# Optimization experiments

Measured on AMD Instinct MI355X. Metric: run time of the kernel, lower is better.

The kernel has to match this reference:

```python
import jax, jax.numpy as jnp
import numpy as np


def setup_inputs() -> dict:
    key = jax.random.key(0)
    kq, kk, kv = jax.random.split(key, 3)
    B, S, D = 4, 4096, 64
    q = jax.random.normal(kq, (B, S, D), dtype=jnp.float32)
    k = jax.random.normal(kk, (B, S, D), dtype=jnp.float32)
    v = jax.random.normal(kv, (B, S, D), dtype=jnp.float32)
    return {"q": q, "k": k, "v": v}


def reference(q, k, v):
    # q,k,v: [B,S,D]. Faithful to the torch module:
    #   attn = softmax(q @ k^T / sqrt(D))  -- softmax over full row (NOT pre-masked)
    #   attn = attn.masked_fill(tril==0, 0.0)  -- post-softmax causal zeroing
    #   out  = attn @ v
    S = q.shape[1]
    d = jnp.sqrt(jnp.asarray(q.shape[-1], dtype=q.dtype))
    scores = jnp.einsum("bqd,bkd->bqk", q, k) / d  # [B,S,S]
    attn = jax.nn.softmax(scores, axis=-1)
    # causal tril mask sliced from the registered buffer mask[:S,:S]
    causal = jnp.tril(jnp.ones((S, S), dtype=bool))  # [S,S]
    attn = jnp.where(causal[None, :, :], attn, jnp.asarray(0.0, dtype=attn.dtype))
    out = jnp.einsum("bqk,bkd->bqd", attn, v)  # [B,S,D]
    return out
```

## Files before the change

### kernel.cpp

```cpp
#include <hip/hip_runtime.h>
#include <math.h>


typedef _Float16 f16;
typedef __attribute__((ext_vector_type(8))) _Float16 f16x8;
typedef __attribute__((ext_vector_type(16))) float f32x16;
typedef __attribute__((ext_vector_type(4))) unsigned int uint4x;

constexpr int S = 4096, D = 64, TK = 32;
constexpr int B_ = 4;
constexpr int NKT = S / TK;
constexpr int WPB = 4;
constexpr int TPW = NKT / WPB;
constexpr float QSC = 0.125f * 1.44269504088896340736f;

__global__ __launch_bounds__(256) void prep(
    const float* __restrict__ K, const float* __restrict__ V,
    f16* __restrict__ Kfrag, f16* __restrict__ Vfrag) {
  const int bx = blockIdx.x, tid = threadIdx.x;
  if (bx < B_ * NKT) {
    const float* src = K + (size_t)bx * TK * D;
    const int key = tid >> 3, j = tid & 7;
    float4 f0 = *reinterpret_cast<const float4*>(src + key * D + j * 8);
    float4 f1 = *reinterpret_cast<const float4*>(src + key * D + j * 8 + 4);
    f16x8 h;
    h[0] = (f16)f0.x; h[1] = (f16)f0.y; h[2] = (f16)f0.z; h[3] = (f16)f0.w;
    h[4] = (f16)f1.x; h[5] = (f16)f1.y; h[6] = (f16)f1.z; h[7] = (f16)f1.w;
    const int kc = j >> 1, h2 = j & 1;
    const int lane = key + 32 * h2;
    *reinterpret_cast<f16x8*>(Kfrag + ((size_t)bx * 4 + kc) * 512 + lane * 8) = h;
  } else {
    __shared__ float t32[TK][D + 4];
    const int vb = bx - B_ * NKT;
    const float* src = V + (size_t)vb * TK * D;
    #pragma unroll
    for (int r = 0; r < 2; ++r) {
      int f4 = tid + r * 256;
      int row = f4 >> 4, c4 = (f4 & 15) * 4;
      *reinterpret_cast<float4*>(&t32[row][c4]) =
          *reinterpret_cast<const float4*>(src + row * D + c4);
    }
    __syncthreads();
    const int dn = tid >> 7, kc2 = (tid >> 6) & 1, lane = tid & 63;
    const int l31 = lane & 31, h2 = lane >> 5;
    const int dim = dn * 32 + l31;
    const int k0 = kc2 * 16 + 8 * h2;
    f16x8 h;
    #pragma unroll
    for (int jj = 0; jj < 8; ++jj) h[jj] = (f16)t32[k0 + jj][dim];
    *reinterpret_cast<f16x8*>(
        Vfrag + ((size_t)vb * 4 + dn * 2 + kc2) * 512 + lane * 8) = h;
  }
}

__global__ __launch_bounds__(256, 3)
void attn(const float* __restrict__ Q, const f16* __restrict__ Kfrag,
          const f16* __restrict__ Vfrag, float* __restrict__ O) {
  __shared__ struct { float nb[2][32][68]; float db[WPB][32]; } sm;

  const int i = blockIdx.x;
  const int b = (i & 7) >> 1;
  const int t = ((i >> 3) << 1) | (i & 1);
  const int qb = (t & 1) ? (127 - (t >> 1)) : (t >> 1);
  const int q0 = qb * TK;

  const int tid = threadIdx.x;
  const int w = tid >> 6, lane = tid & 63;
  const int l31 = lane & 31, h2 = lane >> 5;

  const size_t bSD = (size_t)b * S * D;

  f16x8 qh[4], qlo[4];
  {
    const float* qr = Q + bSD + (size_t)(q0 + l31) * D;
    #pragma unroll
    for (int kc = 0; kc < 4; ++kc) {
      float4 f0 = *reinterpret_cast<const float4*>(qr + kc * 16 + 8 * h2);
      float4 f1 = *reinterpret_cast<const float4*>(qr + kc * 16 + 8 * h2 + 4);
      float f[8] = {f0.x, f0.y, f0.z, f0.w, f1.x, f1.y, f1.z, f1.w};
      #pragma unroll
      for (int j = 0; j < 8; ++j) {
        float v = f[j] * QSC;
        f16 hi = (f16)v;
        qh[kc][j] = hi;
        qlo[kc][j] = (f16)(v - (float)hi);
      }
    }
  }

  const f16* kf = Kfrag + (size_t)b * NKT * 2048 + lane * 8;
  const f16* vf = Vfrag + (size_t)b * NKT * 2048 + lane * 8;

  f32x16 on0, on1;
  float dv[4];
  #pragma unroll
  for (int r = 0; r < 16; ++r) { on0[r] = 0.f; on1[r] = 0.f; }
  #pragma unroll
  for (int r = 0; r < 4; ++r) dv[r] = 0.f;

  f16x8 bk0, bk1, bk2, bk3;
  {
    const f16* kp = kf + (size_t)w * 2048;
    bk0 = *reinterpret_cast<const f16x8*>(kp);
    bk1 = *reinterpret_cast<const f16x8*>(kp + 512);
    bk2 = *reinterpret_cast<const f16x8*>(kp + 1024);
    bk3 = *reinterpret_cast<const f16x8*>(kp + 1536);
  }

  for (int j = 0; j < TPW; ++j) {
    const int kt = (j << 2) | w;
    const int kbase = kt * TK;
    const bool pv = (kbase <= q0);
    const bool diag = (kbase == q0);

    f16x8 v00, v01, v10, v11;
    if (pv) {
      const f16* vp = vf + (size_t)kt * 2048;
      v00 = *reinterpret_cast<const f16x8*>(vp);
      v01 = *reinterpret_cast<const f16x8*>(vp + 512);
      v10 = *reinterpret_cast<const f16x8*>(vp + 1024);
      v11 = *reinterpret_cast<const f16x8*>(vp + 1536);
    }

    f16x8 kn0, kn1, kn2, kn3;
    if (j + 1 < TPW) {
      const f16* kpn = kf + ((size_t)kt + 4) * 2048;
      kn0 = *reinterpret_cast<const f16x8*>(kpn);
      kn1 = *reinterpret_cast<const f16x8*>(kpn + 512);
      kn2 = *reinterpret_cast<const f16x8*>(kpn + 1024);
      kn3 = *reinterpret_cast<const f16x8*>(kpn + 1536);
    }

    f32x16 acc;
    #pragma unroll
    for (int r = 0; r < 16; ++r) acc[r] = 0.f;
    acc = __builtin_amdgcn_mfma_f32_32x32x16_f16(bk0, qlo[0], acc, 0, 0, 0);
    acc = __builtin_amdgcn_mfma_f32_32x32x16_f16(bk0, qh[0],  acc, 0, 0, 0);
    acc = __builtin_amdgcn_mfma_f32_32x32x16_f16(bk1, qlo[1], acc, 0, 0, 0);
    acc = __builtin_amdgcn_mfma_f32_32x32x16_f16(bk1, qh[1],  acc, 0, 0, 0);
    acc = __builtin_amdgcn_mfma_f32_32x32x16_f16(bk2, qlo[2], acc, 0, 0, 0);
    acc = __builtin_amdgcn_mfma_f32_32x32x16_f16(bk2, qh[2],  acc, 0, 0, 0);
    acc = __builtin_amdgcn_mfma_f32_32x32x16_f16(bk3, qlo[3], acc, 0, 0, 0);
    acc = __builtin_amdgcn_mfma_f32_32x32x16_f16(bk3, qh[3],  acc, 0, 0, 0);

    if (pv) {
      unsigned pw[8];
      const int kb4 = 4 * h2;
      #pragma unroll
      for (int i2 = 0; i2 < 8; ++i2) {
        const int ra = 2 * i2, rb = ra + 1;
        float pa = __builtin_amdgcn_exp2f(acc[ra]);
        float pb = __builtin_amdgcn_exp2f(acc[rb]);
        f16 ha = (f16)pa, hb = (f16)pb;
        dv[i2 & 3] += (float)ha + (float)hb;
        unsigned short ba = __builtin_bit_cast(unsigned short, ha);
        unsigned short bb = __builtin_bit_cast(unsigned short, hb);
        if (diag) {
          const int kra = (ra & 3) + 8 * (ra >> 2) + kb4;
          const int krb = (rb & 3) + 8 * (rb >> 2) + kb4;
          ba = (kra <= l31) ? ba : (unsigned short)0;
          bb = (krb <= l31) ? bb : (unsigned short)0;
        }
        pw[i2] = (unsigned)ba | ((unsigned)bb << 16);
      }
      asm("v_permlane32_swap_b32 %0, %1" : "+v"(pw[0]), "+v"(pw[2]));
      asm("v_permlane32_swap_b32 %0, %1" : "+v"(pw[1]), "+v"(pw[3]));
      asm("v_permlane32_swap_b32 %0, %1" : "+v"(pw[4]), "+v"(pw[6]));
      asm("v_permlane32_swap_b32 %0, %1" : "+v"(pw[5]), "+v"(pw[7]));
      uint4x u0 = {pw[0], pw[1], pw[2], pw[3]};
      uint4x u1 = {pw[4], pw[5], pw[6], pw[7]};
      f16x8 ap0 = __builtin_bit_cast(f16x8, u0);
      f16x8 ap1 = __builtin_bit_cast(f16x8, u1);

      on0 = __builtin_amdgcn_mfma_f32_32x32x16_f16(ap0, v00, on0, 0, 0, 0);
      on0 = __builtin_amdgcn_mfma_f32_32x32x16_f16(ap1, v01, on0, 0, 0, 0);
      on1 = __builtin_amdgcn_mfma_f32_32x32x16_f16(ap0, v10, on1, 0, 0, 0);
      on1 = __builtin_amdgcn_mfma_f32_32x32x16_f16(ap1, v11, on1, 0, 0, 0);
    } else {
      #pragma unroll
      for (int r = 0; r < 16; ++r) dv[r & 3] += __builtin_amdgcn_exp2f(acc[r]);
    }

    bk0 = kn0; bk1 = kn1; bk2 = kn2; bk3 = kn3;
  }

  float den = dv[0] + dv[1] + dv[2] + dv[3];
  den += __shfl_xor(den, 32);
  if (h2 == 0) sm.db[w][l31] = den;

  if (w < 2) {
    #pragma unroll
    for (int r = 0; r < 16; ++r) {
      const int row = (r & 3) + 8 * (r >> 2) + 4 * h2;
      sm.nb[w][row][l31]      = on0[r];
      sm.nb[w][row][32 + l31] = on1[r];
    }
  }
  __syncthreads();
  if (w >= 2) {
    #pragma unroll
    for (int r = 0; r < 16; ++r) {
      const int row = (r & 3) + 8 * (r >> 2) + 4 * h2;
      sm.nb[w - 2][row][l31]      += on0[r];
      sm.nb[w - 2][row][32 + l31] += on1[r];
    }
  }
  __syncthreads();

  #pragma unroll
  for (int it = 0; it < 2; ++it) {
    const int i4 = tid + it * 256;
    const int row = i4 >> 4, c4 = (i4 & 15) * 4;
    float dsum = 0.f;
    #pragma unroll
    for (int ww = 0; ww < WPB; ++ww) dsum += sm.db[ww][row];
    const float inv = 1.f / dsum;
    float4 a0 = *reinterpret_cast<const float4*>(&sm.nb[0][row][c4]);
    float4 a1 = *reinterpret_cast<const float4*>(&sm.nb[1][row][c4]);
    float4 o;
    o.x = (a0.x + a1.x) * inv;
    o.y = (a0.y + a1.y) * inv;
    o.z = (a0.z + a1.z) * inv;
    o.w = (a0.w + a1.w) * inv;
    *reinterpret_cast<float4*>(O + bSD + (size_t)(q0 + row) * D + c4) = o;
  }
}

extern "C" void kernel_launch(void* const* d_in, const int* in_sizes, int n_in,
                              void* d_out, int out_size, void* d_ws, size_t ws_size,
                              hipStream_t stream) {
  const float* q = (const float*)d_in[0];
  const float* k = (const float*)d_in[1];
  const float* v = (const float*)d_in[2];
  float* o = (float*)d_out;

  f16* Kfrag = (f16*)d_ws;
  f16* Vfrag = Kfrag + (size_t)B_ * S * D;

  prep<<<dim3(2 * B_ * NKT), dim3(256), 0, stream>>>(k, v, Kfrag, Vfrag);
  attn<<<dim3(512), dim3(256), 0, stream>>>(q, Kfrag, Vfrag, o);
}
```

Measured before the change: 94.22 us.

## Pair early and late query tiles per block so K/V fragments are shared

Each block now handles two query tiles, qb and 127-qb, with 8 waves of 64 lanes instead of 4. Each loaded K/V fragment feeds both tiles' QK^T and PV MFMAs, which halves K/V global traffic per query and balances causal work inside each block. The cost is doubled accumulator registers, a 512-thread launch bound with 2 blocks per CU, only 256 blocks, and a longer shared-memory reduction epilogue with extra barriers.

```diff
diff --git a/kernel.cpp b/kernel.cpp
--- a/kernel.cpp
+++ b/kernel.cpp
@@ -10,7 +10,7 @@
 constexpr int S = 4096, D = 64, TK = 32;
 constexpr int B_ = 4;
 constexpr int NKT = S / TK;
-constexpr int WPB = 4;
+constexpr int WPB = 8;
 constexpr int TPW = NKT / WPB;
 constexpr float QSC = 0.125f * 1.44269504088896340736f;
 
@@ -53,25 +53,31 @@
   }
 }
 
-__global__ __launch_bounds__(256, 3)
+__global__ __launch_bounds__(512, 2)
 void attn(const float* __restrict__ Q, const f16* __restrict__ Kfrag,
           const f16* __restrict__ Vfrag, float* __restrict__ O) {
-  __shared__ struct { float nb[2][32][68]; float db[WPB][32]; } sm;
+  __shared__ struct {
+    float nb[4][32][68];
+    float db[2][8][32];
+  } sm;
 
   const int i = blockIdx.x;
   const int b = (i & 7) >> 1;
-  const int t = ((i >> 3) << 1) | (i & 1);
-  const int qb = (t & 1) ? (127 - (t >> 1)) : (t >> 1);
-  const int q0 = qb * TK;
+  const int qb = ((i >> 3) << 1) | (i & 1);
+  const int qbB = 127 - qb;
+  const int q0A = qb * TK, q0B = qbB * TK;
 
   const int tid = threadIdx.x;
   const int w = tid >> 6, lane = tid & 63;
   const int l31 = lane & 31, h2 = lane >> 5;
+  const int kb4 = 4 * h2;
 
   const size_t bSD = (size_t)b * S * D;
 
-  f16x8 qh[4], qlo[4];
-  {
+  f16x8 qh[2][4], qlo[2][4];
+  #pragma unroll
+  for (int t = 0; t < 2; ++t) {
+    const int q0 = t ? q0B : q0A;
     const float* qr = Q + bSD + (size_t)(q0 + l31) * D;
     #pragma unroll
     for (int kc = 0; kc < 4; ++kc) {
@@ -82,8 +88,8 @@
       for (int j = 0; j < 8; ++j) {
         float v = f[j] * QSC;
         f16 hi = (f16)v;
-        qh[kc][j] = hi;
-        qlo[kc][j] = (f16)(v - (float)hi);
+        qh[t][kc][j] = hi;
+        qlo[t][kc][j] = (f16)(v - (float)hi);
       }
     }
   }
@@ -91,12 +97,50 @@
   const f16* kf = Kfrag + (size_t)b * NKT * 2048 + lane * 8;
   const f16* vf = Vfrag + (size_t)b * NKT * 2048 + lane * 8;
 
-  f32x16 on0, on1;
-  float dv[4];
+  f32x16 onA0, onA1, onB0, onB1;
+  float dvA[4], dvB[4];
   #pragma unroll
-  for (int r = 0; r < 16; ++r) { on0[r] = 0.f; on1[r] = 0.f; }
+  for (int r = 0; r < 16; ++r) {
+    onA0[r] = 0.f; onA1[r] = 0.f; onB0[r] = 0.f; onB1[r] = 0.f;
+  }
   #pragma unroll
-  for (int r = 0; r < 4; ++r) dv[r] = 0.f;
+  for (int r = 0; r < 4; ++r) { dvA[r] = 0.f; dvB[r] = 0.f; }
+
+  auto sm_pv = [&](const f32x16& acc, bool diag, float* dv,
+                   f32x16& o0, f32x16& o1,
+                   const f16x8& v00, const f16x8& v01,
+                   const f16x8& v10, const f16x8& v11) {
+    unsigned pw[8];
+    #pragma unroll
+    for (int i2 = 0; i2 < 8; ++i2) {
+      const int ra = 2 * i2, rb = ra + 1;
+      float pa = __builtin_amdgcn_exp2f(acc[ra]);
+      float pb = __builtin_amdgcn_exp2f(acc[rb]);
+      f16 ha = (f16)pa, hb = (f16)pb;
+      dv[i2 & 3] += (float)ha + (float)hb;
+      unsigned short ba = __builtin_bit_cast(unsigned short, ha);
+      unsigned short bb = __builtin_bit_cast(unsigned short, hb);
+      if (diag) {
+        const int kra = (ra & 3) + 8 * (ra >> 2) + kb4;
+        const int krb = (rb & 3) + 8 * (rb >> 2) + kb4;
+        ba = (kra <= l31) ? ba : (unsigned short)0;
+        bb = (krb <= l31) ? bb : (unsigned short)0;
+      }
+      pw[i2] = (unsigned)ba | ((unsigned)bb << 16);
+    }
+    asm("v_permlane32_swap_b32 %0, %1" : "+v"(pw[0]), "+v"(pw[2]));
+    asm("v_permlane32_swap_b32 %0, %1" : "+v"(pw[1]), "+v"(pw[3]));
+    asm("v_permlane32_swap_b32 %0, %1" : "+v"(pw[4]), "+v"(pw[6]));
+    asm("v_permlane32_swap_b32 %0, %1" : "+v"(pw[5]), "+v"(pw[7]));
+    uint4x u0 = {pw[0], pw[1], pw[2], pw[3]};
+    uint4x u1 = {pw[4], pw[5], pw[6], pw[7]};
+    f16x8 ap0 = __builtin_bit_cast(f16x8, u0);
+    f16x8 ap1 = __builtin_bit_cast(f16x8, u1);
+    o0 = __builtin_amdgcn_mfma_f32_32x32x16_f16(ap0, v00, o0, 0, 0, 0);
+    o0 = __builtin_amdgcn_mfma_f32_32x32x16_f16(ap1, v01, o0, 0, 0, 0);
+    o1 = __builtin_amdgcn_mfma_f32_32x32x16_f16(ap0, v10, o1, 0, 0, 0);
+    o1 = __builtin_amdgcn_mfma_f32_32x32x16_f16(ap1, v11, o1, 0, 0, 0);
+  };
 
   f16x8 bk0, bk1, bk2, bk3;
   {
@@ -108,13 +152,12 @@
   }
 
   for (int j = 0; j < TPW; ++j) {
-    const int kt = (j << 2) | w;
-    const int kbase = kt * TK;
-    const bool pv = (kbase <= q0);
-    const bool diag = (kbase == q0);
+    const int kt = (j << 3) | w;
+    const bool pvA = (kt <= qb),  diagA = (kt == qb);
+    const bool pvB = (kt <= qbB), diagB = (kt == qbB);
 
     f16x8 v00, v01, v10, v11;
-    if (pv) {
+    if (pvB) {
       const f16* vp = vf + (size_t)kt * 2048;
       v00 = *reinterpret_cast<const f16x8*>(vp);
       v01 = *reinterpret_cast<const f16x8*>(vp + 512);
@@ -124,105 +167,133 @@
 
     f16x8 kn0, kn1, kn2, kn3;
     if (j + 1 < TPW) {
-      const f16* kpn = kf + ((size_t)kt + 4) * 2048;
+      const f16* kpn = kf + ((size_t)kt + WPB) * 2048;
       kn0 = *reinterpret_cast<const f16x8*>(kpn);
       kn1 = *reinterpret_cast<const f16x8*>(kpn + 512);
       kn2 = *reinterpret_cast<const f16x8*>(kpn + 1024);
       kn3 = *reinterpret_cast<const f16x8*>(kpn + 1536);
     }
 
-    f32x16 acc;
-    #pragma unroll
-    for (int r = 0; r < 16; ++r) acc[r] = 0.f;
-    acc = __builtin_amdgcn_mfma_f32_32x32x16_f16(bk0, qlo[0], acc, 0, 0, 0);
-    acc = __builtin_amdgcn_mfma_f32_32x32x16_f16(bk0, qh[0],  acc, 0, 0, 0);
-    acc = __builtin_amdgcn_mfma_f32_32x32x16_f16(bk1, qlo[1], acc, 0, 0, 0);
-    acc = __builtin_amdgcn_mfma_f32_32x32x16_f16(bk1, qh[1],  acc, 0, 0, 0);
-    acc = __builtin_amdgcn_mfma_f32_32x32x16_f16(bk2, qlo[2], acc, 0, 0, 0);
-    acc = __builtin_amdgcn_mfma_f32_32x32x16_f16(bk2, qh[2],  acc, 0, 0, 0);
-    acc = __builtin_amdgcn_mfma_f32_32x32x16_f16(bk3, qlo[3], acc, 0, 0, 0);
-    acc = __builtin_amdgcn_mfma_f32_32x32x16_f16(bk3, qh[3],  acc, 0, 0, 0);
-
-    if (pv) {
-      unsigned pw[8];
-      const int kb4 = 4 * h2;
+    {
+      f32x16 acc;
       #pragma unroll
-      for (int i2 = 0; i2 < 8; ++i2) {
-        const int ra = 2 * i2, rb = ra + 1;
-        float pa = __builtin_amdgcn_exp2f(acc[ra]);
-        float pb = __builtin_amdgcn_exp2f(acc[rb]);
-        f16 ha = (f16)pa, hb = (f16)pb;
-        dv[i2 & 3] += (float)ha + (float)hb;
-        unsigned short ba = __builtin_bit_cast(unsigned short, ha);
-        unsigned short bb = __builtin_bit_cast(unsigned short, hb);
-        if (diag) {
-          const int kra = (ra & 3) + 8 * (ra >> 2) + kb4;
-          const int krb = (rb & 3) + 8 * (rb >> 2) + kb4;
-          ba = (kra <= l31) ? ba : (unsigned short)0;
-          bb = (krb <= l31) ? bb : (unsigned short)0;
-        }
-        pw[i2] = (unsigned)ba | ((unsigned)bb << 16);
+      for (int r = 0; r < 16; ++r) acc[r] = 0.f;
+      acc = __builtin_amdgcn_mfma_f32_32x32x16_f16(bk0, qlo[0][0], acc, 0, 0, 0);
+      acc = __builtin_amdgcn_mfma_f32_32x32x16_f16(bk0, qh[0][0],  acc, 0, 0, 0);
+      acc = __builtin_amdgcn_mfma_f32_32x32x16_f16(bk1, qlo[0][1], acc, 0, 0, 0);
+      acc = __builtin_amdgcn_mfma_f32_32x32x16_f16(bk1, qh[0][1],  acc, 0, 0, 0);
+      acc = __builtin_amdgcn_mfma_f32_32x32x16_f16(bk2, qlo[0][2], acc, 0, 0, 0);
+      acc = __builtin_amdgcn_mfma_f32_32x32x16_f16(bk2, qh[0][2],  acc, 0, 0, 0);
+      acc = __builtin_amdgcn_mfma_f32_32x32x16_f16(bk3, qlo[0][3], acc, 0, 0, 0);
+      acc = __builtin_amdgcn_mfma_f32_32x32x16_f16(bk3, qh[0][3],  acc, 0, 0, 0);
+      if (pvA) {
+        sm_pv(acc, diagA, dvA, onA0, onA1, v00, v01, v10, v11);
+      } else {
+        #pragma unroll
+        for (int r = 0; r < 16; ++r) dvA[r & 3] += __builtin_amdgcn_exp2f(acc[r]);
       }
-      asm("v_permlane32_swap_b32 %0, %1" : "+v"(pw[0]), "+v"(pw[2]));
-      asm("v_permlane32_swap_b32 %0, %1" : "+v"(pw[1]), "+v"(pw[3]));
-      asm("v_permlane32_swap_b32 %0, %1" : "+v"(pw[4]), "+v"(pw[6]));
-      asm("v_permlane32_swap_b32 %0, %1" : "+v"(pw[5]), "+v"(pw[7]));
-      uint4x u0 = {pw[0], pw[1], pw[2], pw[3]};
-      uint4x u1 = {pw[4], pw[5], pw[6], pw[7]};
-      f16x8 ap0 = __builtin_bit_cast(f16x8, u0);
-      f16x8 ap1 = __builtin_bit_cast(f16x8, u1);
-
-      on0 = __builtin_amdgcn_mfma_f32_32x32x16_f16(ap0, v00, on0, 0, 0, 0);
-      on0 = __builtin_amdgcn_mfma_f32_32x32x16_f16(ap1, v01, on0, 0, 0, 0);
-      on1 = __builtin_amdgcn_mfma_f32_32x32x16_f16(ap0, v10, on1, 0, 0, 0);
-      on1 = __builtin_amdgcn_mfma_f32_32x32x16_f16(ap1, v11, on1, 0, 0, 0);
-    } else {
+    }
+
+    {
+      f32x16 acc;
       #pragma unroll
-      for (int r = 0; r < 16; ++r) dv[r & 3] += __builtin_amdgcn_exp2f(acc[r]);
+      for (int r = 0; r < 16; ++r) acc[r] = 0.f;
+      acc = __builtin_amdgcn_mfma_f32_32x32x16_f16(bk0, qlo[1][0], acc, 0, 0, 0);
+      acc = __builtin_amdgcn_mfma_f32_32x32x16_f16(bk0, qh[1][0],  acc, 0, 0, 0);
+      acc = __builtin_amdgcn_mfma_f32_32x32x16_f16(bk1, qlo[1][1], acc, 0, 0, 0);
+      acc = __builtin_amdgcn_mfma_f32_32x32x16_f16(bk1, qh[1][1],  acc, 0, 0, 0);
+      acc = __builtin_amdgcn_mfma_f32_32x32x16_f16(bk2, qlo[1][2], acc, 0, 0, 0);
+      acc = __builtin_amdgcn_mfma_f32_32x32x16_f16(bk2, qh[1][2],  acc, 0, 0, 0);
+      acc = __builtin_amdgcn_mfma_f32_32x32x16_f16(bk3, qlo[1][3], acc, 0, 0, 0);
+      acc = __builtin_amdgcn_mfma_f32_32x32x16_f16(bk3, qh[1][3],  acc, 0, 0, 0);
+      if (pvB) {
+        sm_pv(acc, diagB, dvB, onB0, onB1, v00, v01, v10, v11);
+      } else {
+        #pragma unroll
+        for (int r = 0; r < 16; ++r) dvB[r & 3] += __builtin_amdgcn_exp2f(acc[r]);
+      }
     }
 
     bk0 = kn0; bk1 = kn1; bk2 = kn2; bk3 = kn3;
   }
 
-  float den = dv[0] + dv[1] + dv[2] + dv[3];
-  den += __shfl_xor(den, 32);
-  if (h2 == 0) sm.db[w][l31] = den;
-
-  if (w < 2) {
+  float denA = dvA[0] + dvA[1] + dvA[2] + dvA[3];
+  denA += __shfl_xor(denA, 32);
+  float denB = dvB[0] + dvB[1] + dvB[2] + dvB[3];
+  denB += __shfl_xor(denB, 32);
+  if (h2 == 0) { sm.db[0][w][l31] = denA; sm.db[1][w][l31] = denB; }
+
+  if (w < 4) {
     #pragma unroll
     for (int r = 0; r < 16; ++r) {
       const int row = (r & 3) + 8 * (r >> 2) + 4 * h2;
-      sm.nb[w][row][l31]      = on0[r];
-      sm.nb[w][row][32 + l31] = on1[r];
-    }
-  }
-  __syncthreads();
-  if (w >= 2) {
+      sm.nb[w][row][l31]      = onA0[r];
+      sm.nb[w][row][32 + l31] = onA1[r];
+    }
+  }
+  __syncthreads();
+  if (w >= 4) {
     #pragma unroll
     for (int r = 0; r < 16; ++r) {
       const int row = (r & 3) + 8 * (r >> 2) + 4 * h2;
-      sm.nb[w - 2][row][l31]      += on0[r];
-      sm.nb[w - 2][row][32 + l31] += on1[r];
-    }
-  }
-  __syncthreads();
-
-  #pragma unroll
-  for (int it = 0; it < 2; ++it) {
-    const int i4 = tid + it * 256;
-    const int row = i4 >> 4, c4 = (i4 & 15) * 4;
+      sm.nb[w - 4][row][l31]      += onA0[r];
+      sm.nb[w - 4][row][32 + l31] += onA1[r];
+    }
+  }
+  __syncthreads();
+  {
+    const int row = tid >> 4, c4 = (tid & 15) * 4;
     float dsum = 0.f;
     #pragma unroll
-    for (int ww = 0; ww < WPB; ++ww) dsum += sm.db[ww][row];
+    for (int ww = 0; ww < WPB; ++ww) dsum += sm.db[0][ww][row];
     const float inv = 1.f / dsum;
     float4 a0 = *reinterpret_cast<const float4*>(&sm.nb[0][row][c4]);
     float4 a1 = *reinterpret_cast<const float4*>(&sm.nb[1][row][c4]);
+    float4 a2 = *reinterpret_cast<const float4*>(&sm.nb[2][row][c4]);
+    float4 a3 = *reinterpret_cast<const float4*>(&sm.nb[3][row][c4]);
     float4 o;
-    o.x = (a0.x + a1.x) * inv;
-    o.y = (a0.y + a1.y) * inv;
-    o.z = (a0.z + a1.z) * inv;
-    o.w = (a0.w + a1.w) * inv;
-    *reinterpret_cast<float4*>(O + bSD + (size_t)(q0 + row) * D + c4) = o;
+    o.x = (a0.x + a1.x + a2.x + a3.x) * inv;
+    o.y = (a0.y + a1.y + a2.y + a3.y) * inv;
+    o.z = (a0.z + a1.z + a2.z + a3.z) * inv;
+    o.w = (a0.w + a1.w + a2.w + a3.w) * inv;
+    *reinterpret_cast<float4*>(O + bSD + (size_t)(q0A + row) * D + c4) = o;
+  }
+  __syncthreads();
+
+  if (w < 4) {
+    #pragma unroll
+    for (int r = 0; r < 16; ++r) {
+      const int row = (r & 3) + 8 * (r >> 2) + 4 * h2;
+      sm.nb[w][row][l31]      = onB0[r];
+      sm.nb[w][row][32 + l31] = onB1[r];
+    }
+  }
+  __syncthreads();
+  if (w >= 4) {
+    #pragma unroll
+    for (int r = 0; r < 16; ++r) {
+      const int row = (r & 3) + 8 * (r >> 2) + 4 * h2;
+      sm.nb[w - 4][row][l31]      += onB0[r];
+      sm.nb[w - 4][row][32 + l31] += onB1[r];
+    }
+  }
+  __syncthreads();
+  {
+    const int row = tid >> 4, c4 = (tid & 15) * 4;
+    float dsum = 0.f;
+    #pragma unroll
+    for (int ww = 0; ww < WPB; ++ww) dsum += sm.db[1][ww][row];
+    const float inv = 1.f / dsum;
+    float4 a0 = *reinterpret_cast<const float4*>(&sm.nb[0][row][c4]);
+    float4 a1 = *reinterpret_cast<const float4*>(&sm.nb[1][row][c4]);
+    float4 a2 = *reinterpret_cast<const float4*>(&sm.nb[2][row][c4]);
+    float4 a3 = *reinterpret_cast<const float4*>(&sm.nb[3][row][c4]);
+    float4 o;
+    o.x = (a0.x + a1.x + a2.x + a3.x) * inv;
+    o.y = (a0.y + a1.y + a2.y + a3.y) * inv;
+    o.z = (a0.z + a1.z + a2.z + a3.z) * inv;
+    o.w = (a0.w + a1.w + a2.w + a3.w) * inv;
+    *reinterpret_cast<float4*>(O + bSD + (size_t)(q0B + row) * D + c4) = o;
   }
 }
 
@@ -238,5 +309,5 @@
   f16* Vfrag = Kfrag + (size_t)B_ * S * D;
 
   prep<<<dim3(2 * B_ * NKT), dim3(256), 0, stream>>>(k, v, Kfrag, Vfrag);
-  attn<<<dim3(512), dim3(256), 0, stream>>>(q, Kfrag, Vfrag, o);
+  attn<<<dim3(256), dim3(512), 0, stream>>>(q, Kfrag, Vfrag, o);
 }
```

New measurement: 91.87 us. 1.03x faster.
